# Kernel tuning notes

Hardware: AMD Instinct MI355X
Metric: run time of the kernel (lower is better)

Reference implementation:

```python
import jax, jax.numpy as jnp
import numpy as np

EMBED = 128
HID1, HID2 = 400, 200
T_STEPS = 30
NUM_LITS, NUM_CLAUSES = 4000, 8000


def _mlp(x, W1, b1, W2, b2, W3, b3):
    h = jax.nn.relu(x @ W1.T + b1)
    h = jax.nn.relu(h @ W2.T + b2)
    return h @ W3.T + b3


def _lstm_cell(x, h, c, Wih, Whh, b):
    gates = x @ Wih.T + h @ Whh.T + b  # [N, 4*EMBED]
    i, f, g, o = jnp.split(gates, 4, axis=-1)
    c2 = jax.nn.sigmoid(f) * c + jax.nn.sigmoid(i) * jnp.tanh(g)
    h2 = jax.nn.sigmoid(o) * jnp.tanh(c2)
    return h2, c2


def setup_inputs() -> dict:
    key = jax.random.key(0)
    ks = iter(jax.random.split(key, 32))

    def lin(fan_out, fan_in):
        s = 1.0 / np.sqrt(fan_in).astype(np.float32)
        W = jax.random.uniform(next(ks), (fan_out, fan_in), minval=-s, maxval=s, dtype=jnp.float32)
        b = jax.random.uniform(next(ks), (fan_out,), minval=-s, maxval=s, dtype=jnp.float32)
        return W, b

    M = (jax.random.uniform(next(ks), (NUM_LITS, NUM_CLAUSES)) < 0.02).astype(jnp.float32)
    L_init = jax.random.normal(next(ks), (EMBED,), dtype=jnp.float32)
    C_init = jax.random.normal(next(ks), (EMBED,), dtype=jnp.float32)

    LC_W1, LC_b1 = lin(HID1, EMBED); LC_W2, LC_b2 = lin(HID2, HID1); LC_W3, LC_b3 = lin(EMBED, HID2)
    CL_W1, CL_b1 = lin(HID1, EMBED); CL_W2, CL_b2 = lin(HID2, HID1); CL_W3, CL_b3 = lin(EMBED, HID2)
    V_W1, V_b1 = lin(HID1, EMBED); V_W2, V_b2 = lin(HID2, HID1); V_W3, V_b3 = lin(1, HID2)

    def lstm_params():
        s = 1.0 / np.sqrt(EMBED).astype(np.float32)
        Wih = jax.random.uniform(next(ks), (4 * EMBED, EMBED), minval=-s, maxval=s, dtype=jnp.float32)
        Whh = jax.random.uniform(next(ks), (4 * EMBED, EMBED), minval=-s, maxval=s, dtype=jnp.float32)
        b = jax.random.uniform(next(ks), (4 * EMBED,), minval=-s, maxval=s, dtype=jnp.float32)
        return Wih, Whh, b

    L_Wih, L_Whh, L_b = lstm_params()
    C_Wih, C_Whh, C_b = lstm_params()

    return {
        "M": M, "L_init": L_init, "C_init": C_init,
        "LC_W1": LC_W1, "LC_b1": LC_b1, "LC_W2": LC_W2, "LC_b2": LC_b2, "LC_W3": LC_W3, "LC_b3": LC_b3,
        "CL_W1": CL_W1, "CL_b1": CL_b1, "CL_W2": CL_W2, "CL_b2": CL_b2, "CL_W3": CL_W3, "CL_b3": CL_b3,
        "L_Wih": L_Wih, "L_Whh": L_Whh, "L_b": L_b,
        "C_Wih": C_Wih, "C_Whh": C_Whh, "C_b": C_b,
        "V_W1": V_W1, "V_b1": V_b1, "V_W2": V_W2, "V_b2": V_b2, "V_W3": V_W3, "V_b3": V_b3,
    }


def reference(M, L_init, C_init,
              LC_W1, LC_b1, LC_W2, LC_b2, LC_W3, LC_b3,
              CL_W1, CL_b1, CL_W2, CL_b2, CL_W3, CL_b3,
              L_Wih, L_Whh, L_b, C_Wih, C_Whh, C_b,
              V_W1, V_b1, V_W2, V_b2, V_W3, V_b3):
    n_lits, n_clauses = M.shape
    Lh = jnp.tile(L_init[None, :], (n_lits, 1))   # literal hidden (h) state
    Ch = jnp.tile(C_init[None, :], (n_clauses, 1))  # clause hidden (h) state
    Lc = jnp.zeros_like(Lh)
    Cc = jnp.zeros_like(Ch)

    def step(carry, _):
        Lh, Lc, Ch, Cc = carry
        # literal -> clause messages
        LC_msgs = M.T @ _mlp(Lh, LC_W1, LC_b1, LC_W2, LC_b2, LC_W3, LC_b3)  # [n_clauses, E]
        Ch2, Cc2 = _lstm_cell(LC_msgs, Ch, Cc, C_Wih, C_Whh, C_b)
        # clause -> literal messages (uses PRE-update clause state, as in the source loop)
        CL_msgs = M @ _mlp(Ch, CL_W1, CL_b1, CL_W2, CL_b2, CL_W3, CL_b3)    # [n_lits, E]
        Lh2, Lc2 = _lstm_cell(CL_msgs, Lh, Lc, L_Wih, L_Whh, L_b)
        return (Lh2, Lc2, Ch2, Cc2), None

    (Lh, Lc, Ch, Cc), _ = jax.lax.scan(step, (Lh, Lc, Ch, Cc), None, length=T_STEPS)

    # compute_logits: per-literal vote -> mean -> logit
    votes = jax.nn.sigmoid(_mlp(Lh, V_W1, V_b1, V_W2, V_b2, V_W3, V_b3))  # [n_lits, 1] in (0,1)
    avg = jnp.mean(votes)
    return jnp.log(avg / (1.0 - avg))
```

## Files before the change

kernel.cpp:

```cpp
#include <hip/hip_runtime.h>

#define NL 4000
#define NC 8000
#define EMB 128
#define ROWC0 4096
#define NRP 12288
#define NRREAL (ROWC0 + NC)
#define TSTEPS 30
#define LCHUNK 80
#define NCHUNK 50

typedef __attribute__((ext_vector_type(8))) short bf16x8;
typedef __attribute__((ext_vector_type(4))) float f32x4;

__device__ __forceinline__ short f2bf(float x) {
    union { float f; unsigned u; } v; v.f = x;
    unsigned r = v.u + 0x7fffu + ((v.u >> 16) & 1u);
    return (short)(r >> 16);
}
__device__ __forceinline__ float bf2f(short s) {
    union { unsigned u; float f; } v; v.u = ((unsigned)(unsigned short)s) << 16;
    return v.f;
}
__device__ __forceinline__ float sigf(float x) { return 1.f / (1.f + expf(-x)); }
__device__ __forceinline__ float2 h2f2(unsigned u) {
    union { unsigned v; _Float16 h[2]; } x; x.v = u;
    return make_float2((float)x.h[0], (float)x.h[1]);
}
__device__ __forceinline__ void gload16(const void* g, void* l) {
    __builtin_amdgcn_global_load_lds(
        (const __attribute__((address_space(1))) unsigned int*)g,
        (__attribute__((address_space(3))) unsigned int*)l, 16, 0, 0);
}

template<int KS, int OUTM, bool TWOA, bool RELU>
__global__ __launch_bounds__(256) void gemm64(
    const short* __restrict__ A1h, const short* __restrict__ A1l,
    const short* __restrict__ A2h, const short* __restrict__ A2l,
    const short* __restrict__ B1hL, const short* __restrict__ B1lL,
    const short* __restrict__ B1hC, const short* __restrict__ B1lC,
    const short* __restrict__ B2hL, const short* __restrict__ B2lL,
    const short* __restrict__ B2hC, const short* __restrict__ B2lC,
    const float* __restrict__ biasL, const float* __restrict__ biasC,
    short* __restrict__ OH, short* __restrict__ OL, float* __restrict__ OF,
    const float* __restrict__ Cold, float* __restrict__ Cnew,
    int Freal, int Fstore)
{
    __shared__ short sAh[4 * 2048];
    __shared__ short sAl[4 * 2048];
    __shared__ short sBh[4 * 2048];
    __shared__ short sBl[4 * 2048];

    const int row0 = blockIdx.y * 64;
    const int c0 = blockIdx.x * 64;
    const bool isC = (row0 >= ROWC0);
    const int t = threadIdx.x;
    const int lane = t & 63;
    const int w = t >> 6;
    const int wr = w >> 1, wc = w & 1;
    const int l15 = lane & 15;

    f32x4 acc[2][2] = {};
    bool first = true;

    const int nph = TWOA ? 2 : 1;
    for (int ph = 0; ph < nph; ++ph) {
        const short* Ah = (TWOA && ph) ? A2h : A1h;
        const short* Al = (TWOA && ph) ? A2l : A1l;
        const short* Bh = (TWOA && ph) ? (isC ? B2hC : B2hL) : (isC ? B1hC : B1hL);
        const short* Bl = (TWOA && ph) ? (isC ? B2lC : B2lL) : (isC ? B1lC : B1lL);

        for (int kc0 = 0; kc0 < KS; kc0 += 128) {
            const int n32 = ((KS - kc0) >> 5) < 4 ? ((KS - kc0) >> 5) : 4;
            if (!first) __syncthreads();
            first = false;
            const int row = t >> 2, slot = t & 3;
#pragma unroll 4
            for (int q = 0; q < n32; ++q) {
                int gk = kc0 + q * 32 + ((slot ^ ((row >> 1) & 3)) << 3);
                size_t ga = (size_t)(row0 + row) * KS + gk;
                size_t gb = (size_t)(c0 + row) * KS + gk;
                gload16(Ah + ga, &sAh[q * 2048 + t * 8]);
                gload16(Al + ga, &sAl[q * 2048 + t * 8]);
                gload16(Bh + gb, &sBh[q * 2048 + t * 8]);
                gload16(Bl + gb, &sBl[q * 2048 + t * 8]);
            }
            asm volatile("s_waitcnt vmcnt(0)" ::: "memory");
            __syncthreads();
#pragma unroll 4
            for (int q = 0; q < n32; ++q) {
                bf16x8 af[2][2], bf[2][2];
#pragma unroll
                for (int s = 0; s < 2; ++s) {
                    int ar = wr * 32 + s * 16 + l15;
                    int aslot = (lane >> 4) ^ ((ar >> 1) & 3);
                    int ai = q * 2048 + ar * 32 + aslot * 8;
                    af[s][0] = *(const bf16x8*)&sAh[ai];
                    af[s][1] = *(const bf16x8*)&sAl[ai];
                    int br = wc * 32 + s * 16 + l15;
                    int bslot = (lane >> 4) ^ ((br >> 1) & 3);
                    int bi = q * 2048 + br * 32 + bslot * 8;
                    bf[s][0] = *(const bf16x8*)&sBh[bi];
                    bf[s][1] = *(const bf16x8*)&sBl[bi];
                }
#pragma unroll
                for (int s = 0; s < 2; ++s)
#pragma unroll
                    for (int u = 0; u < 2; ++u) {
                        acc[s][u] = __builtin_amdgcn_mfma_f32_16x16x32_bf16(af[s][0], bf[u][0], acc[s][u], 0, 0, 0);
                        acc[s][u] = __builtin_amdgcn_mfma_f32_16x16x32_bf16(af[s][0], bf[u][1], acc[s][u], 0, 0, 0);
                        acc[s][u] = __builtin_amdgcn_mfma_f32_16x16x32_bf16(af[s][1], bf[u][0], acc[s][u], 0, 0, 0);
                    }
            }
        }
    }

    if (OUTM != 3) {
#pragma unroll
        for (int u = 0; u < 2; ++u) {
            int col = c0 + wc * 32 + u * 16 + l15;
            if (col >= Fstore) continue;
            float bv = (col < Freal) ? (isC ? biasC[col] : biasL[col]) : 0.f;
#pragma unroll
            for (int s = 0; s < 2; ++s)
#pragma unroll
                for (int j = 0; j < 4; ++j) {
                    int rowo = row0 + wr * 32 + s * 16 + (lane >> 4) * 4 + j;
                    float v = acc[s][u][j] + bv;
                    if (RELU) v = fmaxf(v, 0.f);
                    size_t oi = (size_t)rowo * Fstore + col;
                    if (OUTM == 1) {
                        short h = f2bf(v);
                        OH[oi] = h;
                        OL[oi] = f2bf(v - bf2f(h));
                    } else {
                        ((_Float16*)OF)[oi] = (_Float16)v;
                    }
                }
        }
    } else {
        const int ql = lane & 3;
#pragma unroll
        for (int u = 0; u < 2; ++u) {
            int colp = c0 + wc * 32 + u * 16 + l15;
            int wrr = (colp & 3) * 128 + (colp >> 2);
            float bv = isC ? biasC[wrr] : biasL[wrr];
            int j = colp >> 2;
#pragma unroll
            for (int s = 0; s < 2; ++s) {
                float ii = 0.f, ff = 0.f, gg = 0.f, oo = 0.f;
#pragma unroll
                for (int r2 = 0; r2 < 4; ++r2) {
                    float v0 = acc[s][u][r2] + bv;
                    float x1 = __shfl_xor(v0, 1);
                    float x2 = __shfl_xor(v0, 2);
                    float x3 = __shfl_xor(v0, 3);
                    float iv = (ql == 0) ? v0 : (ql == 1) ? x1 : (ql == 2) ? x2 : x3;
                    float fv = (ql == 0) ? x1 : (ql == 1) ? v0 : (ql == 2) ? x3 : x2;
                    float gv = (ql == 0) ? x2 : (ql == 1) ? x3 : (ql == 2) ? v0 : x1;
                    float ov = (ql == 0) ? x3 : (ql == 1) ? x2 : (ql == 2) ? x1 : v0;
                    if (ql == r2) { ii = iv; ff = fv; gg = gv; oo = ov; }
                }
                int rowo = row0 + wr * 32 + s * 16 + (lane >> 4) * 4 + ql;
                size_t ci = (size_t)rowo * 128 + j;
                float c2 = sigf(ff) * Cold[ci] + sigf(ii) * tanhf(gg);
                float h2 = sigf(oo) * tanhf(c2);
                Cnew[ci] = c2;
                short h = f2bf(h2);
                OH[ci] = h;
                OL[ci] = f2bf(h2 - bf2f(h));
            }
        }
    }
}

__global__ __launch_bounds__(256) void spmm_kernel(
    const int* __restrict__ Lp, const int* __restrict__ Li,
    const int* __restrict__ Tp, const int* __restrict__ Ti,
    const _Float16* __restrict__ X, short* __restrict__ mh, short* __restrict__ ml)
{
    const int r = blockIdx.x * 4 + (threadIdx.x >> 6);
    const int cp = (threadIdx.x & 63) * 2;
    if (r >= NRREAL) return;
    float s0 = 0.f, s1 = 0.f;
    if (r < NL) {
        int b = Lp[r], e = Lp[r + 1];
        int i = b;
        for (; i + 3 < e; i += 4) {
            unsigned u0 = *(const unsigned*)&X[(size_t)(ROWC0 + Li[i]) * EMB + cp];
            unsigned u1 = *(const unsigned*)&X[(size_t)(ROWC0 + Li[i + 1]) * EMB + cp];
            unsigned u2 = *(const unsigned*)&X[(size_t)(ROWC0 + Li[i + 2]) * EMB + cp];
            unsigned u3 = *(const unsigned*)&X[(size_t)(ROWC0 + Li[i + 3]) * EMB + cp];
            float2 v0 = h2f2(u0), v1 = h2f2(u1), v2 = h2f2(u2), v3 = h2f2(u3);
            s0 += v0.x + v1.x + v2.x + v3.x;
            s1 += v0.y + v1.y + v2.y + v3.y;
        }
        for (; i < e; ++i) {
            float2 v = h2f2(*(const unsigned*)&X[(size_t)(ROWC0 + Li[i]) * EMB + cp]);
            s0 += v.x; s1 += v.y;
        }
    } else if (r >= ROWC0) {
        int c = r - ROWC0;
        int b = Tp[c], e = Tp[c + 1];
        int i = b;
        for (; i + 3 < e; i += 4) {
            unsigned u0 = *(const unsigned*)&X[(size_t)Ti[i] * EMB + cp];
            unsigned u1 = *(const unsigned*)&X[(size_t)Ti[i + 1] * EMB + cp];
            unsigned u2 = *(const unsigned*)&X[(size_t)Ti[i + 2] * EMB + cp];
            unsigned u3 = *(const unsigned*)&X[(size_t)Ti[i + 3] * EMB + cp];
            float2 v0 = h2f2(u0), v1 = h2f2(u1), v2 = h2f2(u2), v3 = h2f2(u3);
            s0 += v0.x + v1.x + v2.x + v3.x;
            s1 += v0.y + v1.y + v2.y + v3.y;
        }
        for (; i < e; ++i) {
            float2 v = h2f2(*(const unsigned*)&X[(size_t)Ti[i] * EMB + cp]);
            s0 += v.x; s1 += v.y;
        }
    } else {
        return;
    }
    size_t oi = (size_t)r * EMB + cp;
    short h0 = f2bf(s0), h1 = f2bf(s1);
    *(unsigned*)&mh[oi] = (unsigned)(unsigned short)h0 | ((unsigned)(unsigned short)h1 << 16);
    short l0 = f2bf(s0 - bf2f(h0)), l1 = f2bf(s1 - bf2f(h1));
    *(unsigned*)&ml[oi] = (unsigned)(unsigned short)l0 | ((unsigned)(unsigned short)l1 << 16);
}

__global__ __launch_bounds__(256) void init_states(
    const float* __restrict__ Li, const float* __restrict__ Ci,
    short* __restrict__ Hh, short* __restrict__ Hl, float* __restrict__ C,
    short* __restrict__ msgsH, short* __restrict__ msgsL, float* __restrict__ accum)
{
    size_t idx = (size_t)blockIdx.x * 256 + threadIdx.x;
    if (idx >= (size_t)NRP * EMB) return;
    int r = (int)(idx >> 7);
    int e = (int)(idx & 127);
    float h = 0.f;
    if (r < NL) h = Li[e];
    else if (r >= ROWC0 && r < NRREAL) h = Ci[e];
    short hh = f2bf(h);
    Hh[idx] = hh;
    Hl[idx] = f2bf(h - bf2f(hh));
    C[idx] = 0.f;
    if (r >= NRREAL || (r >= NL && r < ROWC0)) { msgsH[idx] = 0; msgsL[idx] = 0; }
    if (idx == 0) accum[0] = 0.f;
}

struct SplitJobs {
    const float* src[12];
    short* dh[12]; short* dl[12];
    int rows[12], cols[12], prows[12], pcols[12], perm[12];
};

__global__ __launch_bounds__(256) void split_all(SplitJobs J)
{
    int j = blockIdx.y;
    int i = blockIdx.x * 256 + threadIdx.x;
    int pr = J.prows[j], pc = J.pcols[j];
    if (i >= pr * pc) return;
    int pp = i / pc, c = i - pp * pc;
    int r = J.perm[j] ? (((pp & 3) << 7) | (pp >> 2)) : pp;
    float v = (r < J.rows[j] && c < J.cols[j]) ? J.src[j][(size_t)r * J.cols[j] + c] : 0.f;
    short h = f2bf(v);
    J.dh[j][i] = h;
    J.dl[j][i] = f2bf(v - bf2f(h));
}

__global__ __launch_bounds__(256) void count_rows_L(const float* __restrict__ M, int* __restrict__ cnt)
{
    int l = blockIdx.x, t = threadIdx.x;
    int c_ = 0;
    for (int c = t; c < NC; c += 256) c_ += (M[(size_t)l * NC + c] != 0.f) ? 1 : 0;
#pragma unroll
    for (int off = 32; off > 0; off >>= 1) c_ += __shfl_down(c_, off);
    __shared__ int w[4];
    if ((t & 63) == 0) w[t >> 6] = c_;
    __syncthreads();
    if (t == 0) cnt[l] = w[0] + w[1] + w[2] + w[3];
}

__global__ __launch_bounds__(256) void scan_excl(const int* __restrict__ in, int* __restrict__ out, int n)
{
    const int t = threadIdx.x;
    const int per = (n + 255) >> 8;
    __shared__ int part[256];
    int s = 0;
    const int start = t * per;
    for (int i = 0; i < per; ++i) { int idx = start + i; if (idx < n) s += in[idx]; }
    part[t] = s;
    __syncthreads();
    for (int off = 1; off < 256; off <<= 1) {
        int v = (t >= off) ? part[t - off] : 0;
        __syncthreads();
        part[t] += v;
        __syncthreads();
    }
    int run = (t == 0) ? 0 : part[t - 1];
    for (int i = 0; i < per; ++i) {
        int idx = start + i;
        if (idx < n) { out[idx] = run; run += in[idx]; }
    }
    if (t == 255) out[n] = part[255];
}

__global__ __launch_bounds__(256) void fill_L(const float* __restrict__ M,
                                              const int* __restrict__ Lp, int* __restrict__ Lidx)
{
    int l = blockIdx.x, t = threadIdx.x, lane = t & 63, wid = t >> 6;
    __shared__ int wcnt[4];
    __shared__ int base;
    if (t == 0) base = Lp[l];
    __syncthreads();
    for (int c0 = 0; c0 < NC; c0 += 256) {
        int c = c0 + t;
        bool pr = (c < NC) && (M[(size_t)l * NC + c] != 0.f);
        unsigned long long m = __ballot(pr);
        if (lane == 0) wcnt[wid] = (int)__popcll(m);
        __syncthreads();
        int off = base;
        for (int w = 0; w < wid; ++w) off += wcnt[w];
        int rank = (int)__popcll(m & ((1ull << lane) - 1ull));
        if (pr) Lidx[off + rank] = c;
        __syncthreads();
        if (t == 0) base += wcnt[0] + wcnt[1] + wcnt[2] + wcnt[3];
        __syncthreads();
    }
}

__global__ __launch_bounds__(256) void count_T(const float* __restrict__ M, int* __restrict__ cnt2d)
{
    int s = blockIdx.y;
    int c = blockIdx.x * 256 + threadIdx.x;
    if (c >= NC) return;
    int n = 0;
    int l0 = s * LCHUNK, l1 = l0 + LCHUNK;
    for (int l = l0; l < l1; ++l) n += (M[(size_t)l * NC + c] != 0.f) ? 1 : 0;
    cnt2d[(size_t)s * NC + c] = n;
}

__global__ __launch_bounds__(256) void colscan_T(const int* __restrict__ cnt2d,
                                                 int* __restrict__ cum2d, int* __restrict__ cntT)
{
    int c = blockIdx.x * 256 + threadIdx.x;
    if (c >= NC) return;
    int run = 0;
    for (int s = 0; s < NCHUNK; ++s) {
        cum2d[(size_t)s * NC + c] = run;
        run += cnt2d[(size_t)s * NC + c];
    }
    cntT[c] = run;
}

__global__ __launch_bounds__(256) void fill_T(const float* __restrict__ M,
                                              const int* __restrict__ Tp, const int* __restrict__ cum2d,
                                              int* __restrict__ Tidx)
{
    int s = blockIdx.y;
    int c = blockIdx.x * 256 + threadIdx.x;
    if (c >= NC) return;
    int pos = Tp[c] + cum2d[(size_t)s * NC + c];
    int l0 = s * LCHUNK, l1 = l0 + LCHUNK;
    for (int l = l0; l < l1; ++l) {
        if (M[(size_t)l * NC + c] != 0.f) Tidx[pos++] = l;
    }
}

__global__ __launch_bounds__(256) void vote_reduce(
    const short* __restrict__ H2h, const short* __restrict__ H2l,
    const float* __restrict__ W3, const float* __restrict__ b3, float* __restrict__ accum)
{
    int wid = threadIdx.x >> 6, lane = threadIdx.x & 63;
    int r = blockIdx.x * 4 + wid;
    float s = 0.f;
    if (r < NL) {
        const short* xh = &H2h[(size_t)r * 224];
        const short* xl = &H2l[(size_t)r * 224];
        for (int k = lane; k < 200; k += 64) s += (bf2f(xh[k]) + bf2f(xl[k])) * W3[k];
    }
#pragma unroll
    for (int off = 32; off > 0; off >>= 1) s += __shfl_down(s, off);
    if (lane == 0 && r < NL) {
        float v = 1.f / (1.f + expf(-(s + b3[0])));
        atomicAdd(accum, v);
    }
}

__global__ void finalize_logit(const float* __restrict__ accum, float* __restrict__ out)
{
    float avg = accum[0] / (float)NL;
    out[0] = logf(avg / (1.f - avg));
}

extern "C" void kernel_launch(void* const* d_in, const int* in_sizes, int n_in,
                              void* d_out, int out_size, void* d_ws, size_t ws_size,
                              hipStream_t stream)
{
    const float* M      = (const float*)d_in[0];
    const float* L_init = (const float*)d_in[1];
    const float* C_init = (const float*)d_in[2];
    const float* LC_W1 = (const float*)d_in[3];  const float* LC_b1 = (const float*)d_in[4];
    const float* LC_W2 = (const float*)d_in[5];  const float* LC_b2 = (const float*)d_in[6];
    const float* LC_W3 = (const float*)d_in[7];  const float* LC_b3 = (const float*)d_in[8];
    const float* CL_W1 = (const float*)d_in[9];  const float* CL_b1 = (const float*)d_in[10];
    const float* CL_W2 = (const float*)d_in[11]; const float* CL_b2 = (const float*)d_in[12];
    const float* CL_W3 = (const float*)d_in[13]; const float* CL_b3 = (const float*)d_in[14];
    const float* L_Wih = (const float*)d_in[15]; const float* L_Whh = (const float*)d_in[16];
    const float* L_b   = (const float*)d_in[17];
    const float* C_Wih = (const float*)d_in[18]; const float* C_Whh = (const float*)d_in[19];
    const float* C_b   = (const float*)d_in[20];
    const float* V_W1 = (const float*)d_in[21]; const float* V_b1 = (const float*)d_in[22];
    const float* V_W2 = (const float*)d_in[23]; const float* V_b2 = (const float*)d_in[24];
    const float* V_W3 = (const float*)d_in[25]; const float* V_b3 = (const float*)d_in[26];
    float* out = (float*)d_out;

    char* ws = (char*)d_ws;
    size_t off = 0;
    auto alloc = [&](size_t bytes) -> void* {
        void* pt = ws + off;
        off += (bytes + 255) & ~(size_t)255;
        return pt;
    };
    const size_t NE = (size_t)NRP * EMB;
    short* HAh = (short*)alloc(NE * 2); short* HAl = (short*)alloc(NE * 2);
    short* HBh = (short*)alloc(NE * 2); short* HBl = (short*)alloc(NE * 2);
    float* CA = (float*)alloc(NE * 4);  float* CB = (float*)alloc(NE * 4);
    short* msgsH = (short*)alloc(NE * 2); short* msgsL = (short*)alloc(NE * 2);
    _Float16* X = (_Float16*)alloc(NE * 2);
    short* H1h = (short*)alloc((size_t)NRP * 416 * 2); short* H1l = (short*)alloc((size_t)NRP * 416 * 2);
    short* H2h = (short*)alloc((size_t)NRP * 224 * 2); short* H2l = (short*)alloc((size_t)NRP * 224 * 2);
    float* accum = (float*)alloc(256);
    short* W1hL = (short*)alloc(512 * 128 * 2); short* W1lL = (short*)alloc(512 * 128 * 2);
    short* W1hC = (short*)alloc(512 * 128 * 2); short* W1lC = (short*)alloc(512 * 128 * 2);
    short* W2hL = (short*)alloc(256 * 416 * 2); short* W2lL = (short*)alloc(256 * 416 * 2);
    short* W2hC = (short*)alloc(256 * 416 * 2); short* W2lC = (short*)alloc(256 * 416 * 2);
    short* W3hL = (short*)alloc(128 * 224 * 2); short* W3lL = (short*)alloc(128 * 224 * 2);
    short* W3hC = (short*)alloc(128 * 224 * 2); short* W3lC = (short*)alloc(128 * 224 * 2);
    short* WihhL = (short*)alloc(512 * 128 * 2); short* WihlL = (short*)alloc(512 * 128 * 2);
    short* WhhhL = (short*)alloc(512 * 128 * 2); short* WhhlL = (short*)alloc(512 * 128 * 2);
    short* WihhC = (short*)alloc(512 * 128 * 2); short* WihlC = (short*)alloc(512 * 128 * 2);
    short* WhhhC = (short*)alloc(512 * 128 * 2); short* WhhlC = (short*)alloc(512 * 128 * 2);
    short* V1h = (short*)alloc(512 * 128 * 2); short* V1l = (short*)alloc(512 * 128 * 2);
    short* V2h = (short*)alloc(256 * 416 * 2); short* V2l = (short*)alloc(256 * 416 * 2);
    int* Lp   = (int*)alloc(4104 * 4);
    int* Tp   = (int*)alloc(8104 * 4);
    int* Lidx = (int*)alloc(1000000 * 4);
    int* Tidx = (int*)alloc(1000000 * 4);
    int* cnt2d = (int*)alloc((size_t)NCHUNK * NC * 4);
    int* cum2d = (int*)alloc((size_t)NCHUNK * NC * 4);
    int* cntL = (int*)alloc(4096 * 4);
    int* cntT = (int*)alloc(8192 * 4);
    (void)ws_size; (void)in_sizes; (void)n_in; (void)out_size;

    count_rows_L<<<NL, 256, 0, stream>>>(M, cntL);
    scan_excl<<<1, 256, 0, stream>>>(cntL, Lp, NL);
    fill_L<<<NL, 256, 0, stream>>>(M, Lp, Lidx);
    {
        dim3 g((NC + 255) / 256, NCHUNK);
        count_T<<<g, 256, 0, stream>>>(M, cnt2d);
        colscan_T<<<(NC + 255) / 256, 256, 0, stream>>>(cnt2d, cum2d, cntT);
        scan_excl<<<1, 256, 0, stream>>>(cntT, Tp, NC);
        fill_T<<<g, 256, 0, stream>>>(M, Tp, cum2d, Tidx);
    }

    SplitJobs Jb{};
    auto setj = [&](int j, const float* s, short* dh, short* dl, int r, int c, int pr, int pc, int pm) {
        Jb.src[j] = s; Jb.dh[j] = dh; Jb.dl[j] = dl;
        Jb.rows[j] = r; Jb.cols[j] = c; Jb.prows[j] = pr; Jb.pcols[j] = pc; Jb.perm[j] = pm;
    };
    setj(0, LC_W1, W1hL, W1lL, 400, 128, 512, 128, 0);
    setj(1, CL_W1, W1hC, W1lC, 400, 128, 512, 128, 0);
    setj(2, LC_W2, W2hL, W2lL, 200, 400, 256, 416, 0);
    setj(3, CL_W2, W2hC, W2lC, 200, 400, 256, 416, 0);
    setj(4, LC_W3, W3hL, W3lL, 128, 200, 128, 224, 0);
    setj(5, CL_W3, W3hC, W3lC, 128, 200, 128, 224, 0);
    setj(6, L_Wih, WihhL, WihlL, 512, 128, 512, 128, 1);
    setj(7, L_Whh, WhhhL, WhhlL, 512, 128, 512, 128, 1);
    setj(8, C_Wih, WihhC, WihlC, 512, 128, 512, 128, 1);
    setj(9, C_Whh, WhhhC, WhhlC, 512, 128, 512, 128, 1);
    setj(10, V_W1, V1h, V1l, 400, 128, 512, 128, 0);
    setj(11, V_W2, V2h, V2l, 200, 400, 256, 416, 0);
    {
        dim3 g((106496 + 255) / 256, 12);
        split_all<<<g, 256, 0, stream>>>(Jb);
    }

    const int nelem_blocks = (int)((NE + 255) / 256);
    init_states<<<nelem_blocks, 256, 0, stream>>>(L_init, C_init, HAh, HAl, CA, msgsH, msgsL, accum);

    short *Hch = HAh, *Hcl = HAl, *Hnh = HBh, *Hnl = HBl;
    float *Ccur = CA, *Cnxt = CB;
    for (int step = 0; step < TSTEPS; ++step) {
        gemm64<128, 1, false, true><<<dim3(7, 192), 256, 0, stream>>>(
            Hch, Hcl, nullptr, nullptr,
            W1hL, W1lL, W1hC, W1lC, nullptr, nullptr, nullptr, nullptr,
            LC_b1, CL_b1, H1h, H1l, nullptr, nullptr, nullptr, 400, 416);
        gemm64<416, 1, false, true><<<dim3(4, 192), 256, 0, stream>>>(
            H1h, H1l, nullptr, nullptr,
            W2hL, W2lL, W2hC, W2lC, nullptr, nullptr, nullptr, nullptr,
            LC_b2, CL_b2, H2h, H2l, nullptr, nullptr, nullptr, 200, 224);
        gemm64<224, 4, false, false><<<dim3(2, 192), 256, 0, stream>>>(
            H2h, H2l, nullptr, nullptr,
            W3hL, W3lL, W3hC, W3lC, nullptr, nullptr, nullptr, nullptr,
            LC_b3, CL_b3, nullptr, nullptr, (float*)X, nullptr, nullptr, 128, 128);
        spmm_kernel<<<(NRREAL + 3) / 4, 256, 0, stream>>>(Lp, Lidx, Tp, Tidx, X, msgsH, msgsL);
        gemm64<128, 3, true, false><<<dim3(8, 192), 256, 0, stream>>>(
            msgsH, msgsL, Hch, Hcl,
            WihhL, WihlL, WihhC, WihlC, WhhhL, WhhlL, WhhhC, WhhlC,
            L_b, C_b, Hnh, Hnl, nullptr, Ccur, Cnxt, 512, 512);
        short* th = Hch; Hch = Hnh; Hnh = th;
        short* tl = Hcl; Hcl = Hnl; Hnl = tl;
        float* tc = Ccur; Ccur = Cnxt; Cnxt = tc;
    }

    gemm64<128, 1, false, true><<<dim3(7, 64), 256, 0, stream>>>(
        Hch, Hcl, nullptr, nullptr,
        V1h, V1l, V1h, V1l, nullptr, nullptr, nullptr, nullptr,
        V_b1, V_b1, H1h, H1l, nullptr, nullptr, nullptr, 400, 416);
    gemm64<416, 1, false, true><<<dim3(4, 64), 256, 0, stream>>>(
        H1h, H1l, nullptr, nullptr,
        V2h, V2l, V2h, V2l, nullptr, nullptr, nullptr, nullptr,
        V_b2, V_b2, H2h, H2l, nullptr, nullptr, nullptr, 200, 224);
    vote_reduce<<<(NL + 3) / 4, 256, 0, stream>>>(H2h, H2l, V_W3, V_b3, accum);
    finalize_logit<<<1, 1, 0, stream>>>(accum, out);
}
```

Measured before the change: 3.565 ms.

## Remap GEMM blocks across XCDs, vectorize SpMM gathers, fuse row counting

```diff
diff --git a/kernel.cpp b/kernel.cpp
--- a/kernel.cpp
+++ b/kernel.cpp
@@ -44,15 +44,18 @@
     const float* __restrict__ biasL, const float* __restrict__ biasC,
     short* __restrict__ OH, short* __restrict__ OL, float* __restrict__ OF,
     const float* __restrict__ Cold, float* __restrict__ Cnew,
-    int Freal, int Fstore)
+    int Freal, int Fstore, int nx)
 {
     __shared__ short sAh[4 * 2048];
     __shared__ short sAl[4 * 2048];
     __shared__ short sBh[4 * 2048];
     __shared__ short sBl[4 * 2048];
 
-    const int row0 = blockIdx.y * 64;
-    const int c0 = blockIdx.x * 64;
+    const int flat = blockIdx.x;
+    const int qx = (int)gridDim.x >> 3;
+    const int wg = (flat & 7) * qx + (flat >> 3);
+    const int row0 = (wg / nx) * 64;
+    const int c0 = (wg % nx) * 64;
     const bool isC = (row0 >= ROWC0);
     const int t = threadIdx.x;
     const int lane = t & 63;
@@ -180,50 +183,56 @@
     const _Float16* __restrict__ X, short* __restrict__ mh, short* __restrict__ ml)
 {
     const int r = blockIdx.x * 4 + (threadIdx.x >> 6);
-    const int cp = (threadIdx.x & 63) * 2;
+    const int lane = threadIdx.x & 63;
+    const int eg = lane >> 4;
+    const int cl = lane & 15;
     if (r >= NRREAL) return;
-    float s0 = 0.f, s1 = 0.f;
-    if (r < NL) {
-        int b = Lp[r], e = Lp[r + 1];
-        int i = b;
-        for (; i + 3 < e; i += 4) {
-            unsigned u0 = *(const unsigned*)&X[(size_t)(ROWC0 + Li[i]) * EMB + cp];
-            unsigned u1 = *(const unsigned*)&X[(size_t)(ROWC0 + Li[i + 1]) * EMB + cp];
-            unsigned u2 = *(const unsigned*)&X[(size_t)(ROWC0 + Li[i + 2]) * EMB + cp];
-            unsigned u3 = *(const unsigned*)&X[(size_t)(ROWC0 + Li[i + 3]) * EMB + cp];
-            float2 v0 = h2f2(u0), v1 = h2f2(u1), v2 = h2f2(u2), v3 = h2f2(u3);
-            s0 += v0.x + v1.x + v2.x + v3.x;
-            s1 += v0.y + v1.y + v2.y + v3.y;
+    const int cp = cl * 8;
+
+    int b, e, base;
+    const int* idx;
+    if (r < NL) { b = Lp[r]; e = Lp[r + 1]; idx = Li; base = ROWC0; }
+    else if (r >= ROWC0) { int c = r - ROWC0; b = Tp[c]; e = Tp[c + 1]; idx = Ti; base = 0; }
+    else return;
+
+    float s0 = 0.f, s1 = 0.f, s2 = 0.f, s3 = 0.f, s4 = 0.f, s5 = 0.f, s6 = 0.f, s7 = 0.f;
+    int i = b + eg;
+    bool has = i < e;
+    uint4 v = make_uint4(0, 0, 0, 0);
+    if (has) v = *(const uint4*)&X[(size_t)(base + idx[i]) * EMB + cp];
+    while (has) {
+        int in_ = i + 4;
+        bool hn = in_ < e;
+        uint4 vn = v;
+        if (hn) vn = *(const uint4*)&X[(size_t)(base + idx[in_]) * EMB + cp];
+        float2 f0 = h2f2(v.x), f1 = h2f2(v.y), f2 = h2f2(v.z), f3 = h2f2(v.w);
+        s0 += f0.x; s1 += f0.y; s2 += f1.x; s3 += f1.y;
+        s4 += f2.x; s5 += f2.y; s6 += f3.x; s7 += f3.y;
+        v = vn; i = in_; has = hn;
+    }
+    s0 += __shfl_xor(s0, 16); s0 += __shfl_xor(s0, 32);
+    s1 += __shfl_xor(s1, 16); s1 += __shfl_xor(s1, 32);
+    s2 += __shfl_xor(s2, 16); s2 += __shfl_xor(s2, 32);
+    s3 += __shfl_xor(s3, 16); s3 += __shfl_xor(s3, 32);
+    s4 += __shfl_xor(s4, 16); s4 += __shfl_xor(s4, 32);
+    s5 += __shfl_xor(s5, 16); s5 += __shfl_xor(s5, 32);
+    s6 += __shfl_xor(s6, 16); s6 += __shfl_xor(s6, 32);
+    s7 += __shfl_xor(s7, 16); s7 += __shfl_xor(s7, 32);
+
+    if (eg == 0) {
+        float sv[8] = { s0, s1, s2, s3, s4, s5, s6, s7 };
+        unsigned hp[4], lp[4];
+#pragma unroll
+        for (int j = 0; j < 4; ++j) {
+            short ha = f2bf(sv[2 * j]), hb = f2bf(sv[2 * j + 1]);
+            hp[j] = (unsigned)(unsigned short)ha | ((unsigned)(unsigned short)hb << 16);
+            short la = f2bf(sv[2 * j] - bf2f(ha)), lb = f2bf(sv[2 * j + 1] - bf2f(hb));
+            lp[j] = (unsigned)(unsigned short)la | ((unsigned)(unsigned short)lb << 16);
         }
-        for (; i < e; ++i) {
-            float2 v = h2f2(*(const unsigned*)&X[(size_t)(ROWC0 + Li[i]) * EMB + cp]);
-            s0 += v.x; s1 += v.y;
-        }
-    } else if (r >= ROWC0) {
-        int c = r - ROWC0;
-        int b = Tp[c], e = Tp[c + 1];
-        int i = b;
-        for (; i + 3 < e; i += 4) {
-            unsigned u0 = *(const unsigned*)&X[(size_t)Ti[i] * EMB + cp];
-            unsigned u1 = *(const unsigned*)&X[(size_t)Ti[i + 1] * EMB + cp];
-            unsigned u2 = *(const unsigned*)&X[(size_t)Ti[i + 2] * EMB + cp];
-            unsigned u3 = *(const unsigned*)&X[(size_t)Ti[i + 3] * EMB + cp];
-            float2 v0 = h2f2(u0), v1 = h2f2(u1), v2 = h2f2(u2), v3 = h2f2(u3);
-            s0 += v0.x + v1.x + v2.x + v3.x;
-            s1 += v0.y + v1.y + v2.y + v3.y;
-        }
-        for (; i < e; ++i) {
-            float2 v = h2f2(*(const unsigned*)&X[(size_t)Ti[i] * EMB + cp]);
-            s0 += v.x; s1 += v.y;
-        }
-    } else {
-        return;
-    }
-    size_t oi = (size_t)r * EMB + cp;
-    short h0 = f2bf(s0), h1 = f2bf(s1);
-    *(unsigned*)&mh[oi] = (unsigned)(unsigned short)h0 | ((unsigned)(unsigned short)h1 << 16);
-    short l0 = f2bf(s0 - bf2f(h0)), l1 = f2bf(s1 - bf2f(h1));
-    *(unsigned*)&ml[oi] = (unsigned)(unsigned short)l0 | ((unsigned)(unsigned short)l1 << 16);
+        size_t oi = (size_t)r * EMB + cp;
+        *(uint4*)&mh[oi] = make_uint4(hp[0], hp[1], hp[2], hp[3]);
+        *(uint4*)&ml[oi] = make_uint4(lp[0], lp[1], lp[2], lp[3]);
+    }
 }
 
 __global__ __launch_bounds__(256) void init_states(
@@ -266,17 +275,20 @@
     J.dl[j][i] = f2bf(v - bf2f(h));
 }
 
-__global__ __launch_bounds__(256) void count_rows_L(const float* __restrict__ M, int* __restrict__ cnt)
-{
-    int l = blockIdx.x, t = threadIdx.x;
-    int c_ = 0;
-    for (int c = t; c < NC; c += 256) c_ += (M[(size_t)l * NC + c] != 0.f) ? 1 : 0;
-#pragma unroll
-    for (int off = 32; off > 0; off >>= 1) c_ += __shfl_down(c_, off);
-    __shared__ int w[4];
-    if ((t & 63) == 0) w[t >> 6] = c_;
-    __syncthreads();
-    if (t == 0) cnt[l] = w[0] + w[1] + w[2] + w[3];
+__global__ __launch_bounds__(256) void count_T(const float* __restrict__ M,
+                                               int* __restrict__ cnt2d, int* __restrict__ cntL)
+{
+    int s = blockIdx.y;
+    int c = blockIdx.x * 256 + threadIdx.x;
+    if (c >= NC) return;
+    int n = 0;
+    int l0 = s * LCHUNK, l1 = l0 + LCHUNK;
+    for (int l = l0; l < l1; ++l) {
+        bool nz = M[(size_t)l * NC + c] != 0.f;
+        n += nz ? 1 : 0;
+        if (nz) atomicAdd(&cntL[l], 1);
+    }
+    cnt2d[(size_t)s * NC + c] = n;
 }
 
 __global__ __launch_bounds__(256) void scan_excl(const int* __restrict__ in, int* __restrict__ out, int n)
@@ -325,17 +337,6 @@
         if (t == 0) base += wcnt[0] + wcnt[1] + wcnt[2] + wcnt[3];
         __syncthreads();
     }
-}
-
-__global__ __launch_bounds__(256) void count_T(const float* __restrict__ M, int* __restrict__ cnt2d)
-{
-    int s = blockIdx.y;
-    int c = blockIdx.x * 256 + threadIdx.x;
-    if (c >= NC) return;
-    int n = 0;
-    int l0 = s * LCHUNK, l1 = l0 + LCHUNK;
-    for (int l = l0; l < l1; ++l) n += (M[(size_t)l * NC + c] != 0.f) ? 1 : 0;
-    cnt2d[(size_t)s * NC + c] = n;
 }
 
 __global__ __launch_bounds__(256) void colscan_T(const int* __restrict__ cnt2d,
@@ -451,14 +452,14 @@
     int* cntT = (int*)alloc(8192 * 4);
     (void)ws_size; (void)in_sizes; (void)n_in; (void)out_size;
 
-    count_rows_L<<<NL, 256, 0, stream>>>(M, cntL);
-    scan_excl<<<1, 256, 0, stream>>>(cntL, Lp, NL);
-    fill_L<<<NL, 256, 0, stream>>>(M, Lp, Lidx);
+    hipMemsetAsync(cntL, 0, 4096 * 4, stream);
     {
         dim3 g((NC + 255) / 256, NCHUNK);
-        count_T<<<g, 256, 0, stream>>>(M, cnt2d);
+        count_T<<<g, 256, 0, stream>>>(M, cnt2d, cntL);
         colscan_T<<<(NC + 255) / 256, 256, 0, stream>>>(cnt2d, cum2d, cntT);
         scan_excl<<<1, 256, 0, stream>>>(cntT, Tp, NC);
+        scan_excl<<<1, 256, 0, stream>>>(cntL, Lp, NL);
+        fill_L<<<NL, 256, 0, stream>>>(M, Lp, Lidx);
         fill_T<<<g, 256, 0, stream>>>(M, Tp, cum2d, Tidx);
     }
 
@@ -490,36 +491,36 @@
     short *Hch = HAh, *Hcl = HAl, *Hnh = HBh, *Hnl = HBl;
     float *Ccur = CA, *Cnxt = CB;
     for (int step = 0; step < TSTEPS; ++step) {
-        gemm64<128, 1, false, true><<<dim3(7, 192), 256, 0, stream>>>(
+        gemm64<128, 1, false, true><<<7 * 192, 256, 0, stream>>>(
             Hch, Hcl, nullptr, nullptr,
             W1hL, W1lL, W1hC, W1lC, nullptr, nullptr, nullptr, nullptr,
-            LC_b1, CL_b1, H1h, H1l, nullptr, nullptr, nullptr, 400, 416);
-        gemm64<416, 1, false, true><<<dim3(4, 192), 256, 0, stream>>>(
+            LC_b1, CL_b1, H1h, H1l, nullptr, nullptr, nullptr, 400, 416, 7);
+        gemm64<416, 1, false, true><<<4 * 192, 256, 0, stream>>>(
             H1h, H1l, nullptr, nullptr,
             W2hL, W2lL, W2hC, W2lC, nullptr, nullptr, nullptr, nullptr,
-            LC_b2, CL_b2, H2h, H2l, nullptr, nullptr, nullptr, 200, 224);
-        gemm64<224, 4, false, false><<<dim3(2, 192), 256, 0, stream>>>(
+            LC_b2, CL_b2, H2h, H2l, nullptr, nullptr, nullptr, 200, 224, 4);
+        gemm64<224, 4, false, false><<<2 * 192, 256, 0, stream>>>(
             H2h, H2l, nullptr, nullptr,
             W3hL, W3lL, W3hC, W3lC, nullptr, nullptr, nullptr, nullptr,
-            LC_b3, CL_b3, nullptr, nullptr, (float*)X, nullptr, nullptr, 128, 128);
+            LC_b3, CL_b3, nullptr, nullptr, (float*)X, nullptr, nullptr, 128, 128, 2);
         spmm_kernel<<<(NRREAL + 3) / 4, 256, 0, stream>>>(Lp, Lidx, Tp, Tidx, X, msgsH, msgsL);
-        gemm64<128, 3, true, false><<<dim3(8, 192), 256, 0, stream>>>(
+        gemm64<128, 3, true, false><<<8 * 192, 256, 0, stream>>>(
             msgsH, msgsL, Hch, Hcl,
             WihhL, WihlL, WihhC, WihlC, WhhhL, WhhlL, WhhhC, WhhlC,
-            L_b, C_b, Hnh, Hnl, nullptr, Ccur, Cnxt, 512, 512);
+            L_b, C_b, Hnh, Hnl, nullptr, Ccur, Cnxt, 512, 512, 8);
         short* th = Hch; Hch = Hnh; Hnh = th;
         short* tl = Hcl; Hcl = Hnl; Hnl = tl;
         float* tc = Ccur; Ccur = Cnxt; Cnxt = tc;
     }
 
-    gemm64<128, 1, false, true><<<dim3(7, 64), 256, 0, stream>>>(
+    gemm64<128, 1, false, true><<<7 * 64, 256, 0, stream>>>(
         Hch, Hcl, nullptr, nullptr,
         V1h, V1l, V1h, V1l, nullptr, nullptr, nullptr, nullptr,
-        V_b1, V_b1, H1h, H1l, nullptr, nullptr, nullptr, 400, 416);
-    gemm64<416, 1, false, true><<<dim3(4, 64), 256, 0, stream>>>(
+        V_b1, V_b1, H1h, H1l, nullptr, nullptr, nullptr, 400, 416, 7);
+    gemm64<416, 1, false, true><<<4 * 64, 256, 0, stream>>>(
         H1h, H1l, nullptr, nullptr,
         V2h, V2l, V2h, V2l, nullptr, nullptr, nullptr, nullptr,
-        V_b2, V_b2, H2h, H2l, nullptr, nullptr, nullptr, 200, 224);
+        V_b2, V_b2, H2h, H2l, nullptr, nullptr, nullptr, 200, 224, 4);
     vote_reduce<<<(NL + 3) / 4, 256, 0, stream>>>(H2h, H2l, V_W3, V_b3, accum);
     finalize_logit<<<1, 1, 0, stream>>>(accum, out);
 }
```

New measurement: 3.056 ms. 14.3% less time.
